# Kernel tuning notes

Hardware: AMD Instinct MI355X
Metric: run time of the kernel (lower is better)

The kernel has to match this reference:

```python
import jax, jax.numpy as jnp
import numpy as np

B, N, D, H = 8, 1024, 1024, 16
HEAD_DIM = D // H
SCALING = HEAD_DIM ** (-0.5)
NEG = -1000000000.0


def setup_inputs() -> dict:
    key = jax.random.key(0)
    ks = jax.random.split(key, 7)
    x = jax.random.normal(ks[0], (B, N, D), dtype=jnp.float32)
    # variable-length batch: lengths in [N//2, N], mask[b, i] = i < len_b
    lengths = jax.random.randint(ks[1], (B,), N // 2, N + 1)
    mask = jnp.arange(N)[None, :] < lengths[:, None]  # [B, N] bool
    s = D ** (-0.5)
    Wk = jax.random.normal(ks[2], (D, D), dtype=jnp.float32) * s
    Wq = jax.random.normal(ks[3], (D, D), dtype=jnp.float32) * s
    Wv = jax.random.normal(ks[4], (D, D), dtype=jnp.float32) * s
    Wo = jax.random.normal(ks[5], (D, D), dtype=jnp.float32) * s
    bo = jnp.zeros((D,), dtype=jnp.float32)
    return {"x": x, "mask": mask, "Wk": Wk, "Wq": Wq, "Wv": Wv, "Wo": Wo, "bo": bo}


def reference(x, mask, Wk, Wq, Wv, Wo, bo):
    # torch nn.Linear: y = x @ W.T
    keys = (x @ Wk.T).reshape(B, N, H, HEAD_DIM)
    queries = (x @ Wq.T).reshape(B, N, H, HEAD_DIM)
    values = (x @ Wv.T).reshape(B, N, H, HEAD_DIM)
    # NOTE: faithful to source: keys on i, queries on j, softmax over j
    scores = jnp.einsum('bihx,bjhx->bhij', keys, queries) * SCALING  # [B,H,N,N]
    pair_mask = mask[:, None, :] & mask[:, :, None]                  # [B,N,N]
    scores = scores + jnp.where(pair_mask, 0.0, NEG)[:, None, :, :]
    attn = jax.nn.softmax(scores, axis=-1)
    out = jnp.einsum('bhij,bjhx->bihx', attn, values)                # [B,N,H,hd]
    out = out.reshape(B, N, D)
    out = out @ Wo.T + bo
    # source does out_dense[mask] (ragged); static-shape equivalent: zero padding
    return out * mask[:, :, None].astype(out.dtype)
```

## Files before the change

### kernel.cpp

```cpp
#include <hip/hip_runtime.h>

typedef unsigned short u16;
typedef __attribute__((ext_vector_type(8))) short short8;
typedef __attribute__((ext_vector_type(4))) short short4v;
typedef __attribute__((ext_vector_type(4))) float f32x4;
typedef __attribute__((ext_vector_type(16))) float f32x16;

#define MFMA16(a, b, c) __builtin_amdgcn_mfma_f32_16x16x32_bf16(a, b, c, 0, 0, 0)
#define MFMA32(a, b, c) __builtin_amdgcn_mfma_f32_32x32x16_bf16(a, b, c, 0, 0, 0)

#define BB 8
#define NN 1024
#define DD 1024
#define HH 16
#define HD 64
#define MM (BB * NN)
#define SCLOG2 0.18033688011112042f

static __device__ __forceinline__ u16 f2bf(float f) {
  unsigned u = __float_as_uint(f);
  u += 0x7fffu + ((u >> 16) & 1u);
  return (u16)(u >> 16);
}

static __device__ __forceinline__ void gld16(const void* g, void* l) {
  __builtin_amdgcn_global_load_lds((const __attribute__((address_space(1))) void*)g,
                                   (__attribute__((address_space(3))) void*)l, 16, 0, 0);
}

static __device__ __forceinline__ unsigned cvtpk(float lo, float hi) {
  unsigned r;
  asm("v_cvt_pk_bf16_f32 %0, %1, %2" : "=v"(r) : "v"(lo), "v"(hi));
  return r;
}

static __device__ __forceinline__ f32x16 zero16() {
  f32x16 v;
#pragma unroll
  for (int i = 0; i < 16; ++i) v[i] = 0.f;
  return v;
}

__global__ __launch_bounds__(256) void cast_bf16_kernel(const float* __restrict__ in,
                                                        u16* __restrict__ out, int n8) {
  const int i = blockIdx.x * 256 + threadIdx.x;
  if (i >= n8) return;
  const f32x4* p = (const f32x4*)in + (size_t)i * 2;
  const f32x4 a = p[0], b = p[1];
  short8 o;
  o[0] = (short)f2bf(a[0]); o[1] = (short)f2bf(a[1]);
  o[2] = (short)f2bf(a[2]); o[3] = (short)f2bf(a[3]);
  o[4] = (short)f2bf(b[0]); o[5] = (short)f2bf(b[1]);
  o[6] = (short)f2bf(b[2]); o[7] = (short)f2bf(b[3]);
  *(short8*)(out + (size_t)i * 8) = o;
}

__global__ __launch_bounds__(256) void cast4_lens_kernel(const float* __restrict__ a, const float* __restrict__ b,
                                                         const float* __restrict__ c, const float* __restrict__ d,
                                                         u16* __restrict__ oa, u16* __restrict__ ob,
                                                         u16* __restrict__ oc, u16* __restrict__ od,
                                                         const unsigned char* __restrict__ mask,
                                                         int* __restrict__ lens) {
  if (blockIdx.y == 4) {
    if (blockIdx.x != 0) return;
    __shared__ int acc[BB];
    const int t = threadIdx.x;
    if (t < BB) acc[t] = 0;
    __syncthreads();
    const bool isbyte = (mask[1] != 0);
    for (int bb = 0; bb < BB; ++bb) {
      int s = 0;
      if (isbyte) {
        for (int i = t; i < NN; i += 256) s += mask[(size_t)bb * NN + i] ? 1 : 0;
      } else {
        const int* mi = (const int*)mask;
        for (int i = t; i < NN; i += 256) s += mi[(size_t)bb * NN + i] != 0 ? 1 : 0;
      }
      if (s) atomicAdd(&acc[bb], s);
    }
    __syncthreads();
    if (t < BB) lens[t] = acc[t];
    return;
  }
  const int i = blockIdx.x * 256 + threadIdx.x;
  const float* in;
  u16* out;
  switch (blockIdx.y) {
    case 0: in = a; out = oa; break;
    case 1: in = b; out = ob; break;
    case 2: in = c; out = oc; break;
    default: in = d; out = od; break;
  }
  const f32x4* p = (const f32x4*)in + (size_t)i * 2;
  const f32x4 va = p[0], vb = p[1];
  short8 o;
  o[0] = (short)f2bf(va[0]); o[1] = (short)f2bf(va[1]);
  o[2] = (short)f2bf(va[2]); o[3] = (short)f2bf(va[3]);
  o[4] = (short)f2bf(vb[0]); o[5] = (short)f2bf(vb[1]);
  o[6] = (short)f2bf(vb[2]); o[7] = (short)f2bf(vb[3]);
  *(short8*)(out + (size_t)i * 8) = o;
}

#define STAGE_G(d, k0_)                                                            \
  _Pragma("unroll") for (int p = 0; p < 2; ++p) {                                  \
    const int off = (p * 256 + t) * 16;                                            \
    const int row = off >> 6;                                                      \
    const int colb = (off & 63) ^ (((row >> 1) & 3) << 4);                         \
    gld16(Ag + (size_t)(m0 + row) * 1024 + (k0_) + (colb >> 1), &As[d][off >> 1]); \
    gld16(Bg + (size_t)(n0 + row) * 1024 + (k0_) + (colb >> 1), &Bs[d][off >> 1]); \
  }

#define GEMM_CORE2()                                                            \
  STAGE_G(0, 0)                                                                 \
  __syncthreads();                                                              \
  for (int k0 = 0; k0 < 1024; k0 += 32) {                                       \
    const int cur = (k0 >> 5) & 1;                                              \
    if (k0 + 32 < 1024) { STAGE_G(cur ^ 1, k0 + 32) }                           \
    short8 af[4], bf[4];                                                        \
    _Pragma("unroll") for (int mi = 0; mi < 4; ++mi) {                          \
      const int row = wr * 64 + mi * 16 + li;                                   \
      const int byo = row * 64 + ((lg * 16) ^ (((row >> 1) & 3) << 4));         \
      af[mi] = *(const short8*)((const char*)&As[cur][0] + byo);                \
    }                                                                           \
    _Pragma("unroll") for (int ni = 0; ni < 4; ++ni) {                          \
      const int row = wc * 64 + ni * 16 + li;                                   \
      const int byo = row * 64 + ((lg * 16) ^ (((row >> 1) & 3) << 4));         \
      bf[ni] = *(const short8*)((const char*)&Bs[cur][0] + byo);                \
    }                                                                           \
    __builtin_amdgcn_s_setprio(1);                                              \
    _Pragma("unroll") for (int mi = 0; mi < 4; ++mi)                            \
      _Pragma("unroll") for (int ni = 0; ni < 4; ++ni)                          \
          acc[mi][ni] = MFMA16(af[mi], bf[ni], acc[mi][ni]);                    \
    __builtin_amdgcn_s_setprio(0);                                              \
    __syncthreads();                                                            \
  }

__global__ __launch_bounds__(256) void gemm_qkv(const u16* __restrict__ A,
                                                const u16* __restrict__ Wk3, const u16* __restrict__ Wq3,
                                                const u16* __restrict__ Wv3,
                                                u16* __restrict__ kb, u16* __restrict__ qb,
                                                u16* __restrict__ vtb, const int* __restrict__ lens) {
  const int m0 = blockIdx.x * 128;
  if ((m0 & 1023) >= lens[m0 >> 10]) return;
  __shared__ u16 As[2][4096];
  __shared__ u16 Bs[2][4096];
  const int mat = blockIdx.y >> 3;
  const int n0 = (blockIdx.y & 7) * 128;
  const u16* Ag = A;
  const u16* Bg = (mat == 0) ? Wk3 : (mat == 1) ? Wq3 : Wv3;
  const int t = threadIdx.x;
  const int lane = t & 63;
  const int w = t >> 6;
  const int wr = w >> 1, wc = w & 1;
  const int li = lane & 15, lg = lane >> 4;
  f32x4 acc[4][4] = {};

  GEMM_CORE2()

  if (mat == 2) {
#pragma unroll
    for (int mi = 0; mi < 4; ++mi) {
      const int row = m0 + wr * 64 + mi * 16 + lg * 4;
      const int bb = row >> 10, jj = row & 1023;
#pragma unroll
      for (int ni = 0; ni < 4; ++ni) {
        const int col = n0 + wc * 64 + ni * 16 + li;
        const int h = col >> 6, x = col & 63;
        short4v st;
#pragma unroll
        for (int r = 0; r < 4; ++r) st[r] = (short)f2bf(acc[mi][ni][r]);
        *(short4v*)(vtb + ((size_t)((bb * HH + h) * HD + x)) * NN + jj) = st;
      }
    }
  } else {
    u16* C = (mat == 0) ? kb : qb;
    const float scale = (mat == 0) ? SCLOG2 : 1.0f;
#pragma unroll
    for (int mi = 0; mi < 4; ++mi)
#pragma unroll
      for (int ni = 0; ni < 4; ++ni) {
        const int col = n0 + wc * 64 + ni * 16 + li;
        const int rowb = m0 + wr * 64 + mi * 16 + lg * 4;
#pragma unroll
        for (int r = 0; r < 4; ++r)
          C[(size_t)(rowb + r) * 1024 + col] = f2bf(acc[mi][ni][r] * scale);
      }
  }
}

__global__ __launch_bounds__(256) void gemm_out(const u16* __restrict__ A, const u16* __restrict__ Bw,
                                                float* __restrict__ C, const float* __restrict__ bias,
                                                const int* __restrict__ lens) {
  const int m0 = blockIdx.x * 128;
  const int n0 = blockIdx.y * 128;
  const int t = threadIdx.x;
  if ((m0 & 1023) >= lens[m0 >> 10]) {
    const int r = t >> 1, ch = (t & 1) * 64;
    float* Crow = C + (size_t)(m0 + r) * 1024 + n0 + ch;
    const f32x4 z = {0.f, 0.f, 0.f, 0.f};
#pragma unroll
    for (int c = 0; c < 16; ++c) *(f32x4*)(Crow + c * 4) = z;
    return;
  }
  __shared__ u16 As[2][4096];
  __shared__ u16 Bs[2][4096];
  const u16* Ag = A;
  const u16* Bg = Bw;
  const int lane = t & 63;
  const int w = t >> 6;
  const int wr = w >> 1, wc = w & 1;
  const int li = lane & 15, lg = lane >> 4;
  f32x4 acc[4][4] = {};

  GEMM_CORE2()

#pragma unroll
  for (int ni = 0; ni < 4; ++ni) {
    const int col = n0 + wc * 64 + ni * 16 + li;
    const float bv = bias[col];
#pragma unroll
    for (int mi = 0; mi < 4; ++mi) {
      const int rowb = m0 + wr * 64 + mi * 16 + lg * 4;
#pragma unroll
      for (int r = 0; r < 4; ++r) {
        const int row = rowb + r;
        const int bb = row >> 10, ii = row & 1023;
        const float v = (ii < lens[bb]) ? (acc[mi][ni][r] + bv) : 0.f;
        C[(size_t)row * 1024 + col] = v;
      }
    }
  }
}

__global__ __launch_bounds__(256) void attn_kernel(const u16* __restrict__ Kb, const u16* __restrict__ Qb,
                                                   const u16* __restrict__ Vtb, u16* __restrict__ attb,
                                                   const int* __restrict__ lens) {
  const int bid = blockIdx.x;
  const int b = bid >> 7;
  const int ic = (bid >> 3) & 7;
  const int h = ((bid & 7) << 1) | ((bid >> 6) & 1);
  const int len = lens[b];
  const int i0 = ic * 128;
  if (i0 >= len) return;
  const int t = threadIdx.x;
  const int w = t >> 6, l = t & 63;
  const int l31 = l & 31, hi = l >> 5;
  const int i0w = i0 + w * 32;

  __shared__ u16 Qs[2][4096];
  __shared__ u16 Vs[2][4096];

  short8 kf[4];
  {
    const u16* kp = Kb + ((size_t)(b * NN + i0w + l31)) * DD + h * HD + hi * 8;
#pragma unroll
    for (int ks = 0; ks < 4; ++ks) kf[ks] = *(const short8*)(kp + ks * 16);
  }

  const size_t qsrc = ((size_t)(b * NN) + l31) * DD + h * HD + w * 16 + hi * 8;
  const size_t vsrc = ((size_t)((b * HH + h) * HD + l31)) * NN + w * 16 + hi * 8;

  auto STAGE = [&](int buf, int j0) {
    u16* qd = &Qs[buf][0] + t * 8;
    u16* vd = &Vs[buf][0] + t * 8;
    gld16(Qb + qsrc + (size_t)j0 * DD, qd);
    gld16(Qb + qsrc + (size_t)(j0 + 32) * DD, qd + 2048);
    gld16(Vtb + vsrc + j0, vd);
    gld16(Vtb + vsrc + 32 * NN + j0, vd + 2048);
  };

  f32x16 o0 = zero16(), o1 = zero16();
  float m_run = -3.0e38f, l_run = 0.f;
  const int nt = (len + 63) >> 6;

  STAGE(0, 0);
  __syncthreads();
  for (int jt = 0; jt < nt; ++jt) {
    const int cur = jt & 1;
    const int j0 = jt * 64;
    if (jt + 1 < nt) STAGE(cur ^ 1, j0 + 64);

    const u16* Qc = &Qs[cur][0];
    const u16* Vc = &Vs[cur][0];
    f32x16 s0 = zero16(), s1 = zero16();
    __builtin_amdgcn_s_setprio(1);
#pragma unroll
    for (int ks = 0; ks < 4; ++ks) {
      const short8 qf = *(const short8*)(Qc + (ks * 64 + l) * 8);
      s0 = MFMA32(qf, kf[ks], s0);
    }
#pragma unroll
    for (int ks = 0; ks < 4; ++ks) {
      const short8 qf = *(const short8*)(Qc + ((4 + ks) * 64 + l) * 8);
      s1 = MFMA32(qf, kf[ks], s1);
    }
    __builtin_amdgcn_s_setprio(0);

    if (j0 + 64 > len) {
#pragma unroll
      for (int r = 0; r < 16; ++r) {
        const int jl = (r & 3) + 8 * (r >> 2) + 4 * hi;
        if (j0 + jl >= len) s0[r] = -3.0e38f;
        if (j0 + 32 + jl >= len) s1[r] = -3.0e38f;
      }
    }

    float pmax = s0[0];
#pragma unroll
    for (int r = 1; r < 16; ++r) pmax = fmaxf(pmax, s0[r]);
#pragma unroll
    for (int r = 0; r < 16; ++r) pmax = fmaxf(pmax, s1[r]);
    pmax = fmaxf(pmax, __shfl_xor(pmax, 32));

    if (!__all(pmax <= m_run + 11.5f)) {
      const float mnew = fmaxf(m_run, pmax);
      const float al = __builtin_amdgcn_exp2f(m_run - mnew);
      l_run *= al;
#pragma unroll
      for (int r = 0; r < 16; ++r) { o0[r] *= al; o1[r] *= al; }
      m_run = mnew;
    }

    float rs = 0.f;
#pragma unroll
    for (int r = 0; r < 16; ++r) { const float p = __builtin_amdgcn_exp2f(s0[r] - m_run); s0[r] = p; rs += p; }
#pragma unroll
    for (int r = 0; r < 16; ++r) { const float p = __builtin_amdgcn_exp2f(s1[r] - m_run); s1[r] = p; rs += p; }
    rs += __shfl_xor(rs, 32);
    l_run += rs;

    short8 pf[4];
#pragma unroll
    for (int jk = 0; jk < 4; ++jk) {
      const f32x16& ss = (jk < 2) ? s0 : s1;
      const int kk = jk & 1;
      unsigned W0 = cvtpk(ss[8 * kk + 0], ss[8 * kk + 1]);
      unsigned W1 = cvtpk(ss[8 * kk + 2], ss[8 * kk + 3]);
      unsigned W2 = cvtpk(ss[8 * kk + 4], ss[8 * kk + 5]);
      unsigned W3 = cvtpk(ss[8 * kk + 6], ss[8 * kk + 7]);
      asm("v_permlane32_swap_b32 %0, %1" : "+v"(W0), "+v"(W2));
      asm("v_permlane32_swap_b32 %0, %1" : "+v"(W1), "+v"(W3));
      union { unsigned u[4]; short8 s; } pu;
      pu.u[0] = W0; pu.u[1] = W1; pu.u[2] = W2; pu.u[3] = W3;
      pf[jk] = pu.s;
    }

    __builtin_amdgcn_s_setprio(1);
#pragma unroll
    for (int kkg = 0; kkg < 4; ++kkg) {
      const short8 vf = *(const short8*)(Vc + (kkg * 64 + l) * 8);
      o0 = MFMA32(vf, pf[kkg], o0);
    }
#pragma unroll
    for (int kkg = 0; kkg < 4; ++kkg) {
      const short8 vf = *(const short8*)(Vc + ((4 + kkg) * 64 + l) * 8);
      o1 = MFMA32(vf, pf[kkg], o1);
    }
    __builtin_amdgcn_s_setprio(0);
    __syncthreads();
  }

  const float inv = 1.f / l_run;
  u16* op = attb + (size_t)(b * NN + i0w + l31) * DD + h * HD + hi * 4;
#pragma unroll
  for (int xs = 0; xs < 2; ++xs) {
    const f32x16& oo = xs ? o1 : o0;
#pragma unroll
    for (int q = 0; q < 4; ++q) {
      short4v st;
#pragma unroll
      for (int e = 0; e < 4; ++e) st[e] = (short)f2bf(oo[q * 4 + e] * inv);
      *(short4v*)(op + xs * 32 + q * 8) = st;
    }
  }
}

extern "C" void kernel_launch(void* const* d_in, const int* in_sizes, int n_in,
                              void* d_out, int out_size, void* d_ws, size_t ws_size,
                              hipStream_t stream) {
  const float* x = (const float*)d_in[0];
  const unsigned char* mask = (const unsigned char*)d_in[1];
  const float* Wk = (const float*)d_in[2];
  const float* Wq = (const float*)d_in[3];
  const float* Wv = (const float*)d_in[4];
  const float* Wo = (const float*)d_in[5];
  const float* bo = (const float*)d_in[6];
  float* out = (float*)d_out;

  char* ws = (char*)d_ws;
  size_t o = 0;
  int* lens = (int*)(ws + o); o += 256;
  u16* xb  = (u16*)(ws + o); o += (size_t)MM * DD * 2;
  u16* wkb = (u16*)(ws + o); o += (size_t)DD * DD * 2;
  u16* wqb = (u16*)(ws + o); o += (size_t)DD * DD * 2;
  u16* wvb = (u16*)(ws + o); o += (size_t)DD * DD * 2;
  u16* wob = (u16*)(ws + o); o += (size_t)DD * DD * 2;
  u16* kb  = (u16*)(ws + o); o += (size_t)MM * DD * 2;
  u16* qb  = (u16*)(ws + o); o += (size_t)MM * DD * 2;
  u16* vtb = (u16*)(ws + o); o += (size_t)MM * DD * 2;
  u16* attb = xb;

  const int xn8 = MM * DD / 8;
  cast_bf16_kernel<<<dim3(xn8 / 256), dim3(256), 0, stream>>>(x, xb, xn8);
  cast4_lens_kernel<<<dim3(DD * DD / 8 / 256, 5), dim3(256), 0, stream>>>(
      Wk, Wq, Wv, Wo, wkb, wqb, wvb, wob, mask, lens);

  gemm_qkv<<<dim3(MM / 128, 24), dim3(256), 0, stream>>>(xb, wkb, wqb, wvb, kb, qb, vtb, lens);

  attn_kernel<<<dim3(1024), dim3(256), 0, stream>>>(kb, qb, vtb, attb, lens);

  gemm_out<<<dim3(MM / 128, DD / 128), dim3(256), 0, stream>>>(attb, wob, out, bo, lens);
}
```

Baseline: 184.0 us.

## Software-pipeline attention loop so QK of next tile overlaps softmax/PV

Restructures the flash-attention inner loop into a two-stage software pipeline with ping-pong register sets. Each iteration computes QK^T MFMAs for tile j while running softmax and the PV MFMAs for tile j-1, whose V fragments were already pulled from LDS into registers. Masking is now applied only to the final tile, where it is the only partial one. The aim is to hide exp and transcendental latency behind matrix work, at the cost of roughly doubled score and V-fragment register use, which may lower occupancy or cause spills.

```diff
diff --git a/kernel.cpp b/kernel.cpp
--- a/kernel.cpp
+++ b/kernel.cpp
@@ -232,6 +232,81 @@
   }
 }
 
+#define QK_PART(JC, SN0_, SN1_)                                                \
+  { const u16* Qc = &Qs[(JC) & 1][0];                                          \
+    SN0_ = zero16(); SN1_ = zero16();                                          \
+    __builtin_amdgcn_s_setprio(1);                                             \
+    _Pragma("unroll") for (int ks = 0; ks < 4; ++ks) {                         \
+      const short8 qf = *(const short8*)(Qc + (ks * 64 + l) * 8);              \
+      SN0_ = MFMA32(qf, kf[ks], SN0_); }                                       \
+    _Pragma("unroll") for (int ks = 0; ks < 4; ++ks) {                         \
+      const short8 qf = *(const short8*)(Qc + ((4 + ks) * 64 + l) * 8);        \
+      SN1_ = MFMA32(qf, kf[ks], SN1_); }                                       \
+    __builtin_amdgcn_s_setprio(0); }
+
+#define V_READ(JC, VF_)                                                        \
+  { const u16* Vc = &Vs[(JC) & 1][0];                                          \
+    _Pragma("unroll") for (int kk = 0; kk < 8; ++kk)                           \
+      VF_[kk] = *(const short8*)(Vc + (kk * 64 + l) * 8); }
+
+#define SM_PV(S0_, S1_, VF_)                                                   \
+  {                                                                            \
+    float pmax = S0_[0];                                                       \
+    _Pragma("unroll") for (int r = 1; r < 16; ++r) pmax = fmaxf(pmax, S0_[r]); \
+    _Pragma("unroll") for (int r = 0; r < 16; ++r) pmax = fmaxf(pmax, S1_[r]); \
+    pmax = fmaxf(pmax, __shfl_xor(pmax, 32));                                  \
+    if (!__all(pmax <= m_run + 11.5f)) {                    \
+      const float mnew = fmaxf(m_run, pmax);                                   \
+      const float al = __builtin_amdgcn_exp2f(m_run - mnew);                   \
+      l_run *= al;                                                             \
+      _Pragma("unroll") for (int r = 0; r < 16; ++r) { o0[r] *= al; o1[r] *= al; } \
+      m_run = mnew;                                                            \
+    }                                                                          \
+    float rs = 0.f;                                                            \
+    _Pragma("unroll") for (int r = 0; r < 16; ++r) {                           \
+      const float p = __builtin_amdgcn_exp2f(S0_[r] - m_run); S0_[r] = p; rs += p; } \
+    _Pragma("unroll") for (int r = 0; r < 16; ++r) {                           \
+      const float p = __builtin_amdgcn_exp2f(S1_[r] - m_run); S1_[r] = p; rs += p; } \
+    rs += __shfl_xor(rs, 32);                                                  \
+    l_run += rs;                                                               \
+                     \
+    short8 pf[4];                                                              \
+    _Pragma("unroll") for (int jk = 0; jk < 4; ++jk) {                         \
+      const f32x16& ss = (jk < 2) ? S0_ : S1_;                                 \
+      const int kk2 = jk & 1;                                                  \
+      unsigned W0 = cvtpk(ss[8 * kk2 + 0], ss[8 * kk2 + 1]);                   \
+      unsigned W1 = cvtpk(ss[8 * kk2 + 2], ss[8 * kk2 + 3]);                   \
+      unsigned W2 = cvtpk(ss[8 * kk2 + 4], ss[8 * kk2 + 5]);                   \
+      unsigned W3 = cvtpk(ss[8 * kk2 + 6], ss[8 * kk2 + 7]);                   \
+      asm("v_permlane32_swap_b32 %0, %1" : "+v"(W0), "+v"(W2));                \
+      asm("v_permlane32_swap_b32 %0, %1" : "+v"(W1), "+v"(W3));                \
+      union { unsigned u[4]; short8 s; } pu;                                   \
+      pu.u[0] = W0; pu.u[1] = W1; pu.u[2] = W2; pu.u[3] = W3;                  \
+      pf[jk] = pu.s;                                                           \
+    }                                                                          \
+    __builtin_amdgcn_s_setprio(1);                                             \
+    _Pragma("unroll") for (int kg = 0; kg < 4; ++kg) o0 = MFMA32(VF_[kg], pf[kg], o0); \
+    _Pragma("unroll") for (int kg = 0; kg < 4; ++kg) o1 = MFMA32(VF_[4 + kg], pf[kg], o1); \
+    __builtin_amdgcn_s_setprio(0);                                             \
+  }
+
+#define MASK_LAST(S0_, S1_)                                                    \
+  { const int j0m = (nt - 1) * 64;                                             \
+    if (j0m + 64 > len) {                                                      \
+      _Pragma("unroll") for (int r = 0; r < 16; ++r) {                         \
+        const int jl = (r & 3) + 8 * (r >> 2) + 4 * hi;                        \
+        if (j0m + jl >= len) S0_[r] = -3.0e38f;                                \
+        if (j0m + 32 + jl >= len) S1_[r] = -3.0e38f;                           \
+      } } }
+
+#define ATTN_BODY(JT, SP0, SP1, VFP, SN0, SN1, VFN)                            \
+  { const int jc = (JT);                                                       \
+    if (jc + 1 < nt) STAGE((jc + 1) & 1, (jc + 1) * 64);                       \
+    QK_PART(jc, SN0, SN1)                                                      \
+    SM_PV(SP0, SP1, VFP)                                                       \
+    V_READ(jc, VFN)                                                            \
+    __syncthreads(); }
+
 __global__ __launch_bounds__(256) void attn_kernel(const u16* __restrict__ Kb, const u16* __restrict__ Qb,
                                                    const u16* __restrict__ Vtb, u16* __restrict__ attb,
                                                    const int* __restrict__ lens) {
@@ -273,91 +348,28 @@
   float m_run = -3.0e38f, l_run = 0.f;
   const int nt = (len + 63) >> 6;
 
+  f32x16 sA0, sA1, sB0, sB1;
+  short8 vfA[8], vfB[8];
+
   STAGE(0, 0);
   __syncthreads();
-  for (int jt = 0; jt < nt; ++jt) {
-    const int cur = jt & 1;
-    const int j0 = jt * 64;
-    if (jt + 1 < nt) STAGE(cur ^ 1, j0 + 64);
-
-    const u16* Qc = &Qs[cur][0];
-    const u16* Vc = &Vs[cur][0];
-    f32x16 s0 = zero16(), s1 = zero16();
-    __builtin_amdgcn_s_setprio(1);
-#pragma unroll
-    for (int ks = 0; ks < 4; ++ks) {
-      const short8 qf = *(const short8*)(Qc + (ks * 64 + l) * 8);
-      s0 = MFMA32(qf, kf[ks], s0);
-    }
-#pragma unroll
-    for (int ks = 0; ks < 4; ++ks) {
-      const short8 qf = *(const short8*)(Qc + ((4 + ks) * 64 + l) * 8);
-      s1 = MFMA32(qf, kf[ks], s1);
-    }
-    __builtin_amdgcn_s_setprio(0);
-
-    if (j0 + 64 > len) {
-#pragma unroll
-      for (int r = 0; r < 16; ++r) {
-        const int jl = (r & 3) + 8 * (r >> 2) + 4 * hi;
-        if (j0 + jl >= len) s0[r] = -3.0e38f;
-        if (j0 + 32 + jl >= len) s1[r] = -3.0e38f;
-      }
-    }
-
-    float pmax = s0[0];
-#pragma unroll
-    for (int r = 1; r < 16; ++r) pmax = fmaxf(pmax, s0[r]);
-#pragma unroll
-    for (int r = 0; r < 16; ++r) pmax = fmaxf(pmax, s1[r]);
-    pmax = fmaxf(pmax, __shfl_xor(pmax, 32));
-
-    if (!__all(pmax <= m_run + 11.5f)) {
-      const float mnew = fmaxf(m_run, pmax);
-      const float al = __builtin_amdgcn_exp2f(m_run - mnew);
-      l_run *= al;
-#pragma unroll
-      for (int r = 0; r < 16; ++r) { o0[r] *= al; o1[r] *= al; }
-      m_run = mnew;
-    }
-
-    float rs = 0.f;
-#pragma unroll
-    for (int r = 0; r < 16; ++r) { const float p = __builtin_amdgcn_exp2f(s0[r] - m_run); s0[r] = p; rs += p; }
-#pragma unroll
-    for (int r = 0; r < 16; ++r) { const float p = __builtin_amdgcn_exp2f(s1[r] - m_run); s1[r] = p; rs += p; }
-    rs += __shfl_xor(rs, 32);
-    l_run += rs;
-
-    short8 pf[4];
-#pragma unroll
-    for (int jk = 0; jk < 4; ++jk) {
-      const f32x16& ss = (jk < 2) ? s0 : s1;
-      const int kk = jk & 1;
-      unsigned W0 = cvtpk(ss[8 * kk + 0], ss[8 * kk + 1]);
-      unsigned W1 = cvtpk(ss[8 * kk + 2], ss[8 * kk + 3]);
-      unsigned W2 = cvtpk(ss[8 * kk + 4], ss[8 * kk + 5]);
-      unsigned W3 = cvtpk(ss[8 * kk + 6], ss[8 * kk + 7]);
-      asm("v_permlane32_swap_b32 %0, %1" : "+v"(W0), "+v"(W2));
-      asm("v_permlane32_swap_b32 %0, %1" : "+v"(W1), "+v"(W3));
-      union { unsigned u[4]; short8 s; } pu;
-      pu.u[0] = W0; pu.u[1] = W1; pu.u[2] = W2; pu.u[3] = W3;
-      pf[jk] = pu.s;
-    }
-
-    __builtin_amdgcn_s_setprio(1);
-#pragma unroll
-    for (int kkg = 0; kkg < 4; ++kkg) {
-      const short8 vf = *(const short8*)(Vc + (kkg * 64 + l) * 8);
-      o0 = MFMA32(vf, pf[kkg], o0);
-    }
-#pragma unroll
-    for (int kkg = 0; kkg < 4; ++kkg) {
-      const short8 vf = *(const short8*)(Vc + ((4 + kkg) * 64 + l) * 8);
-      o1 = MFMA32(vf, pf[kkg], o1);
-    }
-    __builtin_amdgcn_s_setprio(0);
-    __syncthreads();
+  if (nt > 1) STAGE(1, 64);
+  QK_PART(0, sA0, sA1)
+  V_READ(0, vfA)
+  __syncthreads();
+
+  int jt = 1;
+  for (; jt + 1 < nt; jt += 2) {
+    ATTN_BODY(jt, sA0, sA1, vfA, sB0, sB1, vfB)
+    ATTN_BODY(jt + 1, sB0, sB1, vfB, sA0, sA1, vfA)
+  }
+  if (jt < nt) {
+    ATTN_BODY(jt, sA0, sA1, vfA, sB0, sB1, vfB)
+    MASK_LAST(sB0, sB1)
+    SM_PV(sB0, sB1, vfB)
+  } else {
+    MASK_LAST(sA0, sA1)
+    SM_PV(sA0, sA1, vfA)
   }
 
   const float inv = 1.f / l_run;
```

New measurement: 180.5 us. Within noise of the previous version (-1.9%).
